# Kernel tuning notes

Hardware: AMD Instinct MI355X
Metric: run time of the kernel (lower is better)

The kernel has to match this reference:

```python
import jax, jax.numpy as jnp
import numpy as np

BS, C_IN, CTX, TGT = 2, 8, 1024, 96
D_MODEL, N_HEADS, D_FF, N_LAYERS = 256, 16, 1024, 4
PF, SF, PC, SC = 8, 4, 32, 16
NF = (CTX + SF - PF) // SF + 1   # 256 fine patches (incl. end-pad)
NC = (CTX + SC - PC) // SC + 1   # 64 coarse patches
TOTAL = NF + NC                  # 320
EPS = 1e-5
DK = D_MODEL // N_HEADS
SCALE = DK ** -0.5


def _patchify(z, plen, stride):
    # ReplicationPad1d((0, stride)) then unfold -> (bs, c, n_patches, plen)
    pad = jnp.broadcast_to(z[..., -1:], z.shape[:-1] + (stride,))
    zp = jnp.concatenate([z, pad], axis=-1)
    n = (zp.shape[-1] - plen) // stride + 1
    idx = np.arange(n)[:, None] * stride + np.arange(plen)[None, :]
    return zp[..., idx]


def _layernorm(x, s, b):
    m = x.mean(-1, keepdims=True)
    v = jnp.var(x, axis=-1, keepdims=True)
    return (x - m) * jax.lax.rsqrt(v + EPS) * s + b


def setup_inputs() -> dict:
    key = jax.random.key(0)
    ks = jax.random.split(key, 16)
    g = lambda k, shape: jax.random.normal(k, shape, jnp.float32) * 0.02
    return {
        "z": jax.random.normal(ks[0], (BS, C_IN, CTX), jnp.float32),
        "revin_w": jnp.ones((C_IN,), jnp.float32),
        "revin_b": jnp.zeros((C_IN,), jnp.float32),
        "Wf": g(ks[1], (PF, D_MODEL)), "bf": jnp.zeros((D_MODEL,), jnp.float32),
        "Wc": g(ks[2], (PC, D_MODEL)), "bc": jnp.zeros((D_MODEL,), jnp.float32),
        "W_pos": jax.random.uniform(ks[3], (TOTAL, D_MODEL), jnp.float32, -0.02, 0.02),
        "WQ": g(ks[4], (N_LAYERS, D_MODEL, D_MODEL)), "bQ": jnp.zeros((N_LAYERS, D_MODEL), jnp.float32),
        "WK": g(ks[5], (N_LAYERS, D_MODEL, D_MODEL)), "bK": jnp.zeros((N_LAYERS, D_MODEL), jnp.float32),
        "WV": g(ks[6], (N_LAYERS, D_MODEL, D_MODEL)), "bV": jnp.zeros((N_LAYERS, D_MODEL), jnp.float32),
        "WO": g(ks[7], (N_LAYERS, D_MODEL, D_MODEL)), "bO": jnp.zeros((N_LAYERS, D_MODEL), jnp.float32),
        "ln1_s": jnp.ones((N_LAYERS, D_MODEL), jnp.float32), "ln1_b": jnp.zeros((N_LAYERS, D_MODEL), jnp.float32),
        "ln2_s": jnp.ones((N_LAYERS, D_MODEL), jnp.float32), "ln2_b": jnp.zeros((N_LAYERS, D_MODEL), jnp.float32),
        "F1": g(ks[8], (N_LAYERS, D_MODEL, D_FF)), "c1": jnp.zeros((N_LAYERS, D_FF), jnp.float32),
        "F2": g(ks[9], (N_LAYERS, D_FF, D_MODEL)), "c2": jnp.zeros((N_LAYERS, D_MODEL), jnp.float32),
        "Wh": g(ks[10], (D_MODEL * TOTAL, TGT)), "bh": jnp.zeros((TGT,), jnp.float32),
    }


def reference(z, revin_w, revin_b, Wf, bf, Wc, bc, W_pos, WQ, bQ, WK, bK, WV, bV,
              WO, bO, ln1_s, ln1_b, ln2_s, ln2_b, F1, c1, F2, c2, Wh, bh):
    # RevIN norm over the time axis (last axis of (bs, c, T))
    mean = z.mean(-1, keepdims=True)
    std = jnp.sqrt(jnp.var(z, axis=-1, keepdims=True) + EPS)
    zn = (z - mean) / std * revin_w[None, :, None] + revin_b[None, :, None]

    # dual-scale patch embedding
    x_fine = _patchify(zn, PF, SF) @ Wf + bf      # (bs, c, NF, d)
    x_coarse = _patchify(zn, PC, SC) @ Wc + bc    # (bs, c, NC, d)
    x = jnp.concatenate([x_fine, x_coarse], axis=2)  # (bs, c, TOTAL, d)

    u = x.reshape(BS * C_IN, TOTAL, D_MODEL) + W_pos  # (B, S, d), B=bs*c

    # residual-score transformer encoder (post-norm)
    prev = None
    for l in range(N_LAYERS):
        q = (u @ WQ[l] + bQ[l]).reshape(-1, TOTAL, N_HEADS, DK).transpose(0, 2, 1, 3)
        k = (u @ WK[l] + bK[l]).reshape(-1, TOTAL, N_HEADS, DK).transpose(0, 2, 1, 3)
        v = (u @ WV[l] + bV[l]).reshape(-1, TOTAL, N_HEADS, DK).transpose(0, 2, 1, 3)
        s = jnp.einsum('bhqd,bhkd->bhqk', q, k) * SCALE
        if prev is not None:
            s = s + prev
        w = jax.nn.softmax(s, axis=-1)
        o = jnp.einsum('bhqk,bhkd->bhqd', w, v).transpose(0, 2, 1, 3).reshape(-1, TOTAL, D_MODEL)
        o = o @ WO[l] + bO[l]
        u = _layernorm(u + o, ln1_s[l], ln1_b[l])
        h = jax.nn.gelu(u @ F1[l] + c1[l], approximate=False) @ F2[l] + c2[l]
        u = _layernorm(u + h, ln2_s[l], ln2_b[l])
        prev = s

    # head: (bs, c, TOTAL, d) -> permute -> flatten(d, TOTAL) -> linear
    zz = u.reshape(BS, C_IN, TOTAL, D_MODEL).transpose(0, 1, 3, 2).reshape(BS, C_IN, D_MODEL * TOTAL)
    out = zz @ Wh + bh  # (bs, c, TGT)

    # RevIN denorm
    out = (out - revin_b[None, :, None]) / (revin_w[None, :, None] + EPS * EPS) * std + mean
    return out
```

## Files before the change

### kernel.cpp

```cpp
#include <hip/hip_runtime.h>
#include <math.h>

typedef unsigned short ushort;
typedef unsigned int uint;
typedef __attribute__((ext_vector_type(8))) short short8;
typedef __attribute__((ext_vector_type(4))) float f32x4;
typedef __attribute__((ext_vector_type(4))) ushort us4;

constexpr int BS = 2, C_IN = 8, CTX = 1024, TGT = 96;
constexpr int DM = 256, NH = 16, DFF = 1024, NL = 4;
constexpr int NF = 256, TOTAL = 320;
constexpr int NB = 16;
constexpr int DK = 16;
constexpr float EPS = 1e-5f;
constexpr float SCALE = 0.25f;
constexpr int KHEAD = DM * TOTAL;
constexpr int M = NB * TOTAL;

__device__ __forceinline__ ushort f2b(float x) {
    uint u = __float_as_uint(x);
    u += 0x7fff + ((u >> 16) & 1);
    return (ushort)(u >> 16);
}
__device__ __forceinline__ float bu2f(ushort x) { return __uint_as_float(((uint)x) << 16); }
__device__ __forceinline__ uint pack2(float a, float b) { return (uint)f2b(a) | ((uint)f2b(b) << 16); }

typedef __attribute__((address_space(3))) uint lds_u32;
typedef const __attribute__((address_space(1))) uint glb_u32;
__device__ __forceinline__ void ldst16(const void* g, void* l) {
    __builtin_amdgcn_global_load_lds((glb_u32*)g, (lds_u32*)l, 16, 0, 0);
}

__global__ void k_prep(const float* __restrict__ WQ, const float* __restrict__ WK,
                       const float* __restrict__ WV, const float* __restrict__ WO,
                       const float* __restrict__ F1, const float* __restrict__ F2,
                       const float* __restrict__ Wh,
                       ushort* __restrict__ Wtqkv, ushort* __restrict__ WtO,
                       ushort* __restrict__ Ft1, ushort* __restrict__ Ft2,
                       ushort* __restrict__ WhT2,
                       const float* __restrict__ z, const float* __restrict__ rw,
                       const float* __restrict__ rb, float* __restrict__ zn,
                       const float* __restrict__ bhv, float* __restrict__ outp,
                       float* __restrict__ scalef) {
    __shared__ ushort tile[32][33];
    __shared__ float rr1[16], rr2[16], bcast[2];
    int i = blockIdx.x;
    int tx = threadIdx.x, ty = threadIdx.y;
    if (i < 1024) {
        int zz = i >> 6, w = zz >> 2, l = zz & 3;
        const float* src = (w == 0 ? WQ : (w == 1 ? WK : (w == 2 ? WV : WO))) + l * 65536;
        ushort* dst = (w < 3) ? (Wtqkv + (size_t)l * 768 * 256 + w * 256 * 256)
                              : (WtO + (size_t)l * 65536);
        int c0 = (i & 7) * 32, r0 = ((i >> 3) & 7) * 32;
        tile[ty][tx] = f2b(src[(r0 + ty) * 256 + c0 + tx]);
        __syncthreads();
        dst[(c0 + ty) * 256 + r0 + tx] = tile[tx][ty];
    } else if (i < 2048) {
        int j = i - 1024, l = j >> 8;
        const float* src = F1 + (size_t)l * 262144;
        ushort* dst = Ft1 + (size_t)l * 262144;
        int c0 = (j & 31) * 32, r0 = ((j >> 5) & 7) * 32;
        tile[ty][tx] = f2b(src[(r0 + ty) * 1024 + c0 + tx]);
        __syncthreads();
        dst[(c0 + ty) * 256 + r0 + tx] = tile[tx][ty];
    } else if (i < 3072) {
        int j = i - 2048, l = j >> 8;
        const float* src = F2 + (size_t)l * 262144;
        ushort* dst = Ft2 + (size_t)l * 262144;
        int c0 = (j & 7) * 32, r0 = ((j >> 3) & 31) * 32;
        tile[ty][tx] = f2b(src[(r0 + ty) * 256 + c0 + tx]);
        __syncthreads();
        dst[(c0 + ty) * 1024 + r0 + tx] = tile[tx][ty];
    } else if (i < 10752) {
        int j = i - 3072;
        int t0 = (j % 3) * 32, rest = j / 3;
        int d0 = (rest & 7) * 32, pp = rest >> 3;
        tile[ty][tx] = f2b(Wh[((size_t)(d0 + ty) * 320 + pp) * 96 + t0 + tx]);
        __syncthreads();
        WhT2[(size_t)(t0 + ty) * KHEAD + pp * 256 + d0 + tx] = tile[tx][ty];
    } else {
        int bc = i - 10752;
        int tid = ty * 32 + tx;
        float x = z[bc * CTX + tid];
        float s1 = x, s2 = x * x;
#pragma unroll
        for (int off = 1; off < 64; off <<= 1) {
            s1 += __shfl_xor(s1, off);
            s2 += __shfl_xor(s2, off);
        }
        if ((tid & 63) == 0) { rr1[tid >> 6] = s1; rr2[tid >> 6] = s2; }
        __syncthreads();
        if (tid == 0) {
            float a1 = 0.f, a2 = 0.f;
            for (int k = 0; k < 16; k++) { a1 += rr1[k]; a2 += rr2[k]; }
            float m = a1 * (1.0f / CTX);
            float var = a2 * (1.0f / CTX) - m * m;
            float sd = sqrtf(var + EPS);
            bcast[0] = m; bcast[1] = sd;
        }
        __syncthreads();
        float m = bcast[0], sd = bcast[1];
        int c = bc & 7;
        float w = rw[c], bb = rb[c];
        zn[bc * CTX + tid] = (x - m) / sd * w + bb;
        if (tid < TGT) outp[bc * TGT + tid] = (bhv[tid] - bb) / (w + EPS * EPS) * sd + m;
        if (tid == 0) scalef[bc] = sd / (w + EPS * EPS);
    }
}

__global__ void k_embed(const float* __restrict__ zn, const float* __restrict__ Wf,
                        const float* __restrict__ bfv, const float* __restrict__ Wc,
                        const float* __restrict__ bcv, const float* __restrict__ Wpos,
                        ushort* __restrict__ u) {
    int bc = blockIdx.x / TOTAL, p = blockIdx.x % TOTAL, d = threadIdx.x;
    float acc;
    if (p < NF) {
        acc = bfv[d];
        int base = p * 4;
        for (int i = 0; i < 8; i++) {
            int idx = min(base + i, CTX - 1);
            acc += zn[bc * CTX + idx] * Wf[i * DM + d];
        }
    } else {
        int pc = p - NF;
        acc = bcv[d];
        int base = pc * 16;
        for (int i = 0; i < 32; i++) {
            int idx = min(base + i, CTX - 1);
            acc += zn[bc * CTX + idx] * Wc[i * DM + d];
        }
    }
    acc += Wpos[p * DM + d];
    u[(bc * TOTAL + p) * DM + d] = f2b(acc);
}

template <int GELU, int QKV>
__global__ __launch_bounds__(256) void k_gemm_mfma(const ushort* __restrict__ A,
                                                   const ushort* __restrict__ Wt,
                                                   const float* __restrict__ b0,
                                                   const float* __restrict__ b1,
                                                   const float* __restrict__ b2,
                                                   ushort* __restrict__ C,
                                                   ushort* __restrict__ C2,
                                                   int Mm, int N, int K) {
    __shared__ ushort As[64][32];
    __shared__ ushort Bs[64][32];
    int tid = threadIdx.x;
    int wave = tid >> 6, lane = tid & 63;
    int quad = lane >> 4, l16 = lane & 15;
    int m0 = blockIdx.y * 64, n0 = blockIdx.x * 64;

    f32x4 acc[4];
#pragma unroll
    for (int nt = 0; nt < 4; nt++) acc[nt] = (f32x4){0.f, 0.f, 0.f, 0.f};

    int srow = wave * 16 + (lane >> 2);
    int sc = (lane & 3) ^ ((srow >> 1) & 3);
    ushort* AsW = &As[wave * 16][0];
    ushort* BsW = &Bs[wave * 16][0];
    const ushort* Ag = &A[(size_t)(m0 + srow) * K + sc * 8];
    const ushort* Bg = &Wt[(size_t)(n0 + srow) * K + sc * 8];
    int rchunk = (quad ^ ((l16 >> 1) & 3)) * 8;

    for (int k0 = 0; k0 < K; k0 += 32) {
        ldst16(Ag + k0, AsW);
        ldst16(Bg + k0, BsW);
        __syncthreads();
        short8 af = *(const short8*)&As[wave * 16 + l16][rchunk];
#pragma unroll
        for (int nt = 0; nt < 4; nt++) {
            short8 bf = *(const short8*)&Bs[nt * 16 + l16][rchunk];
            acc[nt] = __builtin_amdgcn_mfma_f32_16x16x32_bf16(af, bf, acc[nt], 0, 0, 0);
        }
        __syncthreads();
    }
#pragma unroll
    for (int nt = 0; nt < 4; nt++) {
        int col = n0 + nt * 16 + l16;
        float bi;
        if (QKV) {
            int bs = (n0 + nt * 16) >> 8;
            const float* bp = bs == 0 ? b0 : (bs == 1 ? b1 : b2);
            bi = bp[col & 255];
        } else {
            bi = b0[col];
        }
#pragma unroll
        for (int r = 0; r < 4; r++) {
            int rowm = m0 + wave * 16 + quad * 4 + r;
            float vv = acc[nt][r] + bi;
            if (GELU) vv = vv * 0.5f * (1.0f + erff(vv * 0.70710678118f));
            if (QKV) {
                int bs = col >> 8;
                ushort* dst = (bs == 2) ? (C2 + (size_t)rowm * DM)
                                        : (C + (size_t)bs * (M * DM) + (size_t)rowm * DM);
                dst[col & 255] = f2b(vv);
            } else {
                C[(size_t)rowm * N + col] = f2b(vv);
            }
        }
    }
}

__global__ __launch_bounds__(256) void k_gemm_ln16(const ushort* __restrict__ A,
                                                   const ushort* __restrict__ Wt,
                                                   const float* __restrict__ bias,
                                                   const float* __restrict__ ls,
                                                   const float* __restrict__ lb,
                                                   ushort* __restrict__ u, int K) {
    __shared__ ushort As[16][32];
    __shared__ ushort Bs[256][32];
    __shared__ float ps1[16][4], ps2[16][4];
    int tid = threadIdx.x;
    int wave = tid >> 6, lane = tid & 63;
    int quad = lane >> 4, l16 = lane & 15;
    int m0 = blockIdx.x * 16;

    f32x4 acc[4];
#pragma unroll
    for (int nt = 0; nt < 4; nt++) acc[nt] = (f32x4){0.f, 0.f, 0.f, 0.f};

    int brow = wave * 16 + (lane >> 2);
    int bc_swz = (lane & 3) ^ ((brow >> 1) & 3);
    const ushort* Bg0 = &Wt[(size_t)brow * K + bc_swz * 8];
    ushort* BsW0 = &Bs[wave * 16][0];
    int ar = lane >> 2;
    int ac = (lane & 3) ^ ((ar >> 1) & 3);
    const ushort* Ag = &A[(size_t)(m0 + ar) * K + ac * 8];
    int rchunk = (quad ^ ((l16 >> 1) & 3)) * 8;

    for (int k0 = 0; k0 < K; k0 += 32) {
        if (tid < 64) ldst16(Ag + k0, &As[0][0]);
#pragma unroll
        for (int i = 0; i < 4; i++)
            ldst16(Bg0 + (size_t)i * 64 * K + k0, BsW0 + i * 64 * 32);
        __syncthreads();
        short8 af = *(const short8*)&As[l16][rchunk];
#pragma unroll
        for (int nt = 0; nt < 4; nt++) {
            short8 bf = *(const short8*)&Bs[wave * 64 + nt * 16 + l16][rchunk];
            acc[nt] = __builtin_amdgcn_mfma_f32_16x16x32_bf16(af, bf, acc[nt], 0, 0, 0);
        }
        __syncthreads();
    }
    float xv[4][4];
#pragma unroll
    for (int r = 0; r < 4; r++) {
        int rowg = m0 + quad * 4 + r;
        float s1 = 0.f, s2 = 0.f;
#pragma unroll
        for (int nt = 0; nt < 4; nt++) {
            int col = wave * 64 + nt * 16 + l16;
            float x = acc[nt][r] + bias[col] + bu2f(u[(size_t)rowg * DM + col]);
            xv[r][nt] = x; s1 += x; s2 += x * x;
        }
        s1 += __shfl_xor(s1, 1); s2 += __shfl_xor(s2, 1);
        s1 += __shfl_xor(s1, 2); s2 += __shfl_xor(s2, 2);
        s1 += __shfl_xor(s1, 4); s2 += __shfl_xor(s2, 4);
        s1 += __shfl_xor(s1, 8); s2 += __shfl_xor(s2, 8);
        if (l16 == 0) { ps1[quad * 4 + r][wave] = s1; ps2[quad * 4 + r][wave] = s2; }
    }
    __syncthreads();
#pragma unroll
    for (int r = 0; r < 4; r++) {
        int rowl = quad * 4 + r, rowg = m0 + rowl;
        float s1 = ps1[rowl][0] + ps1[rowl][1] + ps1[rowl][2] + ps1[rowl][3];
        float s2 = ps2[rowl][0] + ps2[rowl][1] + ps2[rowl][2] + ps2[rowl][3];
        float m = s1 * (1.0f / DM);
        float var = s2 * (1.0f / DM) - m * m;
        float rs = rsqrtf(var + EPS);
#pragma unroll
        for (int nt = 0; nt < 4; nt++) {
            int col = wave * 64 + nt * 16 + l16;
            u[(size_t)rowg * DM + col] = f2b((xv[r][nt] - m) * rs * ls[col] + lb[col]);
        }
    }
}

__global__ __launch_bounds__(256, 4) void k_attn(const ushort* __restrict__ qk, const ushort* __restrict__ vm,
                                                 ushort* __restrict__ ao, int nj) {
    __shared__ ushort sh[10240];
    uint* sh32 = (uint*)sh;
    int bh = blockIdx.x, b = bh >> 4, h = bh & 15;
    int i0 = blockIdx.y * 64;
    int t = threadIdx.x, wave = t >> 6, lane = t & 63, quad = lane >> 4, l16 = lane & 15;
    const short8 zero8 = (short8){0, 0, 0, 0, 0, 0, 0, 0};

    f32x4 acc[20];
#pragma unroll
    for (int nt = 0; nt < 20; nt++) acc[nt] = (f32x4){0.f, 0.f, 0.f, 0.f};

    for (int idx = t; idx < 320; idx += 256) {
        int jp = idx >> 1, dh = idx & 1;
        int j = jp * 2;
        uint4 a = *(const uint4*)&vm[((size_t)b * TOTAL + j) * DM + h * DK + dh * 8];
        uint4 bb = *(const uint4*)&vm[((size_t)b * TOTAL + j + 1) * DM + h * DK + dh * 8];
        const ushort* ap = (const ushort*)&a;
        const ushort* bp = (const ushort*)&bb;
        int jr = j & 31;
        int q = (jr & 15) >> 2, jj = ((jr >> 4) << 2) + (jr & 3);
        int base = 5120 + ((j >> 5) * 4 + q) * 128 + jj;
#pragma unroll
        for (int dd = 0; dd < 8; dd++) {
            int d = dh * 8 + dd;
            uint val = (uint)ap[dd] | ((uint)bp[dd] << 16);
            sh32[(base + d * 8) >> 1] = val;
        }
    }

    for (int jl = 0; jl < nj; jl++) {
        const ushort* qm = qk + (size_t)(2 * jl) * M * DM;
        const ushort* km = qm + (size_t)M * DM;
        for (int idx = t; idx < 640; idx += 256) {
            int j = idx >> 1, half = idx & 1;
            short8 kv = *(const short8*)&km[((size_t)b * TOTAL + j) * DM + h * DK + half * 8];
            int jt = j >> 4, jln = j & 15;
            *(short8*)&sh[((jt * 2 + half) * 16 + jln) * 8] = kv;
        }
        short8 qf = zero8;
        if (quad < 2) qf = *(const short8*)&qm[((size_t)b * TOTAL + i0 + wave * 16 + l16) * DM + h * DK + quad * 8];
        __syncthreads();
#pragma unroll
        for (int nt = 0; nt < 20; nt++) {
            short8 kf = *(const short8*)&sh[((nt * 2 + (quad & 1)) * 16 + l16) * 8];
            acc[nt] = __builtin_amdgcn_mfma_f32_16x16x32_bf16(kf, qf, acc[nt], 0, 0, 0);
        }
        __syncthreads();
    }

    float mx = -1e30f;
#pragma unroll
    for (int nt = 0; nt < 20; nt++)
#pragma unroll
        for (int r = 0; r < 4; r++) { acc[nt][r] *= SCALE; mx = fmaxf(mx, acc[nt][r]); }
    mx = fmaxf(mx, __shfl_xor(mx, 16));
    mx = fmaxf(mx, __shfl_xor(mx, 32));
    float sum = 0.f;
#pragma unroll
    for (int nt = 0; nt < 20; nt++)
#pragma unroll
        for (int r = 0; r < 4; r++) { acc[nt][r] = __expf(acc[nt][r] - mx); sum += acc[nt][r]; }
    sum += __shfl_xor(sum, 16);
    sum += __shfl_xor(sum, 32);
    float inv = 1.f / sum;
#pragma unroll
    for (int nt = 0; nt < 20; nt++)
#pragma unroll
        for (int r = 0; r < 4; r++) acc[nt][r] *= inv;

    f32x4 oacc = (f32x4){0.f, 0.f, 0.f, 0.f};
#pragma unroll
    for (int jt2 = 0; jt2 < 10; jt2++) {
        short8 vt = *(const short8*)&sh[5120 + ((jt2 * 4 + quad) * 16 + l16) * 8];
        union { short8 v; uint u[4]; } pf;
        pf.u[0] = pack2(acc[2 * jt2][0], acc[2 * jt2][1]);
        pf.u[1] = pack2(acc[2 * jt2][2], acc[2 * jt2][3]);
        pf.u[2] = pack2(acc[2 * jt2 + 1][0], acc[2 * jt2 + 1][1]);
        pf.u[3] = pack2(acc[2 * jt2 + 1][2], acc[2 * jt2 + 1][3]);
        oacc = __builtin_amdgcn_mfma_f32_16x16x32_bf16(vt, pf.v, oacc, 0, 0, 0);
    }
    us4 ov4 = (us4){f2b(oacc[0]), f2b(oacc[1]), f2b(oacc[2]), f2b(oacc[3])};
    *(us4*)&ao[((size_t)b * TOTAL + i0 + wave * 16 + l16) * DM + h * DK + quad * 4] = ov4;
}

__global__ __launch_bounds__(256) void k_head(const ushort* __restrict__ u, const ushort* __restrict__ WhT2,
                                              const float* __restrict__ scalef, float* __restrict__ out) {
    int t0 = blockIdx.x * 16;
    int wave = threadIdx.x >> 6, lane = threadIdx.x & 63;
    int quad = lane >> 4, l16 = lane & 15;
    int chunk = blockIdx.y * 4 + wave;
    int kbeg = chunk * 1024;
    f32x4 acc = (f32x4){0.f, 0.f, 0.f, 0.f};
    const ushort* za = &u[(size_t)l16 * KHEAD + quad * 8];
    const ushort* wb = &WhT2[(size_t)(t0 + l16) * KHEAD + quad * 8];
#pragma unroll 4
    for (int k = kbeg; k < kbeg + 1024; k += 32) {
        short8 af = *(const short8*)&za[k];
        short8 bf = *(const short8*)&wb[k];
        acc = __builtin_amdgcn_mfma_f32_16x16x32_bf16(af, bf, acc, 0, 0, 0);
    }
#pragma unroll
    for (int r = 0; r < 4; r++) {
        int bcr = quad * 4 + r;
        atomicAdd(&out[bcr * TGT + t0 + l16], acc[r] * scalef[bcr]);
    }
}

extern "C" void kernel_launch(void* const* d_in, const int* in_sizes, int n_in,
                              void* d_out, int out_size, void* d_ws, size_t ws_size,
                              hipStream_t stream) {
    const float* z       = (const float*)d_in[0];
    const float* revin_w = (const float*)d_in[1];
    const float* revin_b = (const float*)d_in[2];
    const float* Wf      = (const float*)d_in[3];
    const float* bfv     = (const float*)d_in[4];
    const float* Wc      = (const float*)d_in[5];
    const float* bcv     = (const float*)d_in[6];
    const float* Wpos    = (const float*)d_in[7];
    const float* WQ      = (const float*)d_in[8];
    const float* bQ      = (const float*)d_in[9];
    const float* WK      = (const float*)d_in[10];
    const float* bK      = (const float*)d_in[11];
    const float* WV      = (const float*)d_in[12];
    const float* bV      = (const float*)d_in[13];
    const float* WO      = (const float*)d_in[14];
    const float* bO      = (const float*)d_in[15];
    const float* ln1s    = (const float*)d_in[16];
    const float* ln1b    = (const float*)d_in[17];
    const float* ln2s    = (const float*)d_in[18];
    const float* ln2b    = (const float*)d_in[19];
    const float* F1      = (const float*)d_in[20];
    const float* c1      = (const float*)d_in[21];
    const float* F2      = (const float*)d_in[22];
    const float* c2      = (const float*)d_in[23];
    const float* Wh      = (const float*)d_in[24];
    const float* bh      = (const float*)d_in[25];
    float* out = (float*)d_out;

    char* p = (char*)d_ws;
    float* scalef = (float*)p;   p += 16 * 4;
    p = (char*)(((size_t)p + 255) & ~255ull);
    float* zn = (float*)p;       p += NB * CTX * 4;
    ushort* u     = (ushort*)p;  p += (size_t)M * DM * 2;
    ushort* qkbuf = (ushort*)p;  p += (size_t)NL * 2 * M * DM * 2;
    ushort* vbuf  = (ushort*)p;  p += (size_t)M * DM * 2;
    ushort* ax    = (ushort*)p;  p += (size_t)M * DM * 2;
    ushort* hbuf  = (ushort*)p;  p += (size_t)M * DFF * 2;
    ushort* Wtqkv = (ushort*)p;  p += (size_t)NL * 768 * 256 * 2;
    ushort* WtO   = (ushort*)p;  p += (size_t)NL * 256 * 256 * 2;
    ushort* Ft1   = (ushort*)p;  p += (size_t)NL * 1024 * 256 * 2;
    ushort* Ft2   = (ushort*)p;  p += (size_t)NL * 256 * 1024 * 2;
    ushort* WhT2  = (ushort*)p;  p += (size_t)TGT * KHEAD * 2;

    k_prep<<<10768, dim3(32, 32), 0, stream>>>(WQ, WK, WV, WO, F1, F2, Wh,
                                               Wtqkv, WtO, Ft1, Ft2, WhT2,
                                               z, revin_w, revin_b, zn,
                                               bh, out, scalef);
    k_embed<<<NB * TOTAL, 256, 0, stream>>>(zn, Wf, bfv, Wc, bcv, Wpos, u);

    for (int l = 0; l < NL; l++) {
        k_gemm_mfma<0, 1><<<dim3(12, 80), 256, 0, stream>>>(
            u, Wtqkv + (size_t)l * 768 * 256, bQ + l * DM, bK + l * DM, bV + l * DM,
            qkbuf + (size_t)l * 2 * M * DM, vbuf, M, 768, 256);
        k_attn<<<dim3(NB * NH, 5), 256, 0, stream>>>(qkbuf, vbuf, ax, l + 1);
        k_gemm_ln16<<<M / 16, 256, 0, stream>>>(
            ax, WtO + (size_t)l * 65536, bO + l * DM, ln1s + l * DM, ln1b + l * DM, u, 256);
        k_gemm_mfma<1, 0><<<dim3(16, 80), 256, 0, stream>>>(
            u, Ft1 + (size_t)l * 262144, c1 + l * DFF, c1, c1, hbuf, hbuf, M, 1024, 256);
        k_gemm_ln16<<<M / 16, 256, 0, stream>>>(
            hbuf, Ft2 + (size_t)l * 262144, c2 + l * DM, ln2s + l * DM, ln2b + l * DM, u, 1024);
    }

    k_head<<<dim3(TGT / 16, 20), 256, 0, stream>>>(u, WhT2, scalef, out);
}
```

Baseline: 459.4 us.

## Double-buffer LDS tiles in GEMM kernels and attention K staging

Both MFMA GEMM kernels now use two LDS buffers. The next K-slice is loaded with global_load_lds while the current slice feeds the MFMAs, and each step ends with a single waitcnt+barrier instead of two __syncthreads. The attention kernel alternates K staging between two LDS regions so the trailing barrier per layer-iteration can be dropped. This hides global-load latency and cuts barrier count, at the cost of doubled LDS use, which may reduce occupancy.

```diff
diff --git a/kernel.cpp b/kernel.cpp
--- a/kernel.cpp
+++ b/kernel.cpp
@@ -30,6 +30,8 @@
 __device__ __forceinline__ void ldst16(const void* g, void* l) {
     __builtin_amdgcn_global_load_lds((glb_u32*)g, (lds_u32*)l, 16, 0, 0);
 }
+
+#define PIPE_BARRIER() asm volatile("s_waitcnt vmcnt(0)\n\ts_barrier" ::: "memory")
 
 __global__ void k_prep(const float* __restrict__ WQ, const float* __restrict__ WK,
                        const float* __restrict__ WV, const float* __restrict__ WO,
@@ -143,8 +145,8 @@
                                                    ushort* __restrict__ C,
                                                    ushort* __restrict__ C2,
                                                    int Mm, int N, int K) {
-    __shared__ ushort As[64][32];
-    __shared__ ushort Bs[64][32];
+    __shared__ ushort As[2][64][32];
+    __shared__ ushort Bs[2][64][32];
     int tid = threadIdx.x;
     int wave = tid >> 6, lane = tid & 63;
     int quad = lane >> 4, l16 = lane & 15;
@@ -156,23 +158,29 @@
 
     int srow = wave * 16 + (lane >> 2);
     int sc = (lane & 3) ^ ((srow >> 1) & 3);
-    ushort* AsW = &As[wave * 16][0];
-    ushort* BsW = &Bs[wave * 16][0];
     const ushort* Ag = &A[(size_t)(m0 + srow) * K + sc * 8];
     const ushort* Bg = &Wt[(size_t)(n0 + srow) * K + sc * 8];
     int rchunk = (quad ^ ((l16 >> 1) & 3)) * 8;
 
-    for (int k0 = 0; k0 < K; k0 += 32) {
-        ldst16(Ag + k0, AsW);
-        ldst16(Bg + k0, BsW);
-        __syncthreads();
-        short8 af = *(const short8*)&As[wave * 16 + l16][rchunk];
+    ldst16(Ag, &As[0][wave * 16][0]);
+    ldst16(Bg, &Bs[0][wave * 16][0]);
+    PIPE_BARRIER();
+
+    int nstep = K >> 5;
+    int cur = 0;
+    for (int t = 0; t < nstep; t++) {
+        if (t + 1 < nstep) {
+            ldst16(Ag + (t + 1) * 32, &As[cur ^ 1][wave * 16][0]);
+            ldst16(Bg + (t + 1) * 32, &Bs[cur ^ 1][wave * 16][0]);
+        }
+        short8 af = *(const short8*)&As[cur][wave * 16 + l16][rchunk];
 #pragma unroll
         for (int nt = 0; nt < 4; nt++) {
-            short8 bf = *(const short8*)&Bs[nt * 16 + l16][rchunk];
+            short8 bf = *(const short8*)&Bs[cur][nt * 16 + l16][rchunk];
             acc[nt] = __builtin_amdgcn_mfma_f32_16x16x32_bf16(af, bf, acc[nt], 0, 0, 0);
         }
-        __syncthreads();
+        PIPE_BARRIER();
+        cur ^= 1;
     }
 #pragma unroll
     for (int nt = 0; nt < 4; nt++) {
@@ -208,8 +216,8 @@
                                                    const float* __restrict__ ls,
                                                    const float* __restrict__ lb,
                                                    ushort* __restrict__ u, int K) {
-    __shared__ ushort As[16][32];
-    __shared__ ushort Bs[256][32];
+    __shared__ ushort As[2][16][32];
+    __shared__ ushort Bs[2][256][32];
     __shared__ float ps1[16][4], ps2[16][4];
     int tid = threadIdx.x;
     int wave = tid >> 6, lane = tid & 63;
@@ -223,25 +231,34 @@
     int brow = wave * 16 + (lane >> 2);
     int bc_swz = (lane & 3) ^ ((brow >> 1) & 3);
     const ushort* Bg0 = &Wt[(size_t)brow * K + bc_swz * 8];
-    ushort* BsW0 = &Bs[wave * 16][0];
     int ar = lane >> 2;
     int ac = (lane & 3) ^ ((ar >> 1) & 3);
     const ushort* Ag = &A[(size_t)(m0 + ar) * K + ac * 8];
     int rchunk = (quad ^ ((l16 >> 1) & 3)) * 8;
 
-    for (int k0 = 0; k0 < K; k0 += 32) {
-        if (tid < 64) ldst16(Ag + k0, &As[0][0]);
-#pragma unroll
-        for (int i = 0; i < 4; i++)
-            ldst16(Bg0 + (size_t)i * 64 * K + k0, BsW0 + i * 64 * 32);
-        __syncthreads();
-        short8 af = *(const short8*)&As[l16][rchunk];
+    if (tid < 64) ldst16(Ag, &As[0][0][0]);
+#pragma unroll
+    for (int i = 0; i < 4; i++)
+        ldst16(Bg0 + (size_t)i * 64 * K, &Bs[0][i * 64 + wave * 16][0]);
+    PIPE_BARRIER();
+
+    int nstep = K >> 5;
+    int cur = 0;
+    for (int t = 0; t < nstep; t++) {
+        if (t + 1 < nstep) {
+            if (tid < 64) ldst16(Ag + (t + 1) * 32, &As[cur ^ 1][0][0]);
+#pragma unroll
+            for (int i = 0; i < 4; i++)
+                ldst16(Bg0 + (size_t)i * 64 * K + (t + 1) * 32, &Bs[cur ^ 1][i * 64 + wave * 16][0]);
+        }
+        short8 af = *(const short8*)&As[cur][l16][rchunk];
 #pragma unroll
         for (int nt = 0; nt < 4; nt++) {
-            short8 bf = *(const short8*)&Bs[wave * 64 + nt * 16 + l16][rchunk];
+            short8 bf = *(const short8*)&Bs[cur][wave * 64 + nt * 16 + l16][rchunk];
             acc[nt] = __builtin_amdgcn_mfma_f32_16x16x32_bf16(af, bf, acc[nt], 0, 0, 0);
         }
-        __syncthreads();
+        PIPE_BARRIER();
+        cur ^= 1;
     }
     float xv[4][4];
 #pragma unroll
@@ -279,7 +296,7 @@
 
 __global__ __launch_bounds__(256, 4) void k_attn(const ushort* __restrict__ qk, const ushort* __restrict__ vm,
                                                  ushort* __restrict__ ao, int nj) {
-    __shared__ ushort sh[10240];
+    __shared__ ushort sh[15360];
     uint* sh32 = (uint*)sh;
     int bh = blockIdx.x, b = bh >> 4, h = bh & 15;
     int i0 = blockIdx.y * 64;
@@ -299,7 +316,7 @@
         const ushort* bp = (const ushort*)&bb;
         int jr = j & 31;
         int q = (jr & 15) >> 2, jj = ((jr >> 4) << 2) + (jr & 3);
-        int base = 5120 + ((j >> 5) * 4 + q) * 128 + jj;
+        int base = 10240 + ((j >> 5) * 4 + q) * 128 + jj;
 #pragma unroll
         for (int dd = 0; dd < 8; dd++) {
             int d = dh * 8 + dd;
@@ -311,21 +328,21 @@
     for (int jl = 0; jl < nj; jl++) {
         const ushort* qm = qk + (size_t)(2 * jl) * M * DM;
         const ushort* km = qm + (size_t)M * DM;
+        int kb = (jl & 1) * 5120;
         for (int idx = t; idx < 640; idx += 256) {
             int j = idx >> 1, half = idx & 1;
             short8 kv = *(const short8*)&km[((size_t)b * TOTAL + j) * DM + h * DK + half * 8];
             int jt = j >> 4, jln = j & 15;
-            *(short8*)&sh[((jt * 2 + half) * 16 + jln) * 8] = kv;
+            *(short8*)&sh[kb + ((jt * 2 + half) * 16 + jln) * 8] = kv;
         }
         short8 qf = zero8;
         if (quad < 2) qf = *(const short8*)&qm[((size_t)b * TOTAL + i0 + wave * 16 + l16) * DM + h * DK + quad * 8];
         __syncthreads();
 #pragma unroll
         for (int nt = 0; nt < 20; nt++) {
-            short8 kf = *(const short8*)&sh[((nt * 2 + (quad & 1)) * 16 + l16) * 8];
+            short8 kf = *(const short8*)&sh[kb + ((nt * 2 + (quad & 1)) * 16 + l16) * 8];
             acc[nt] = __builtin_amdgcn_mfma_f32_16x16x32_bf16(kf, qf, acc[nt], 0, 0, 0);
         }
-        __syncthreads();
     }
 
     float mx = -1e30f;
@@ -351,7 +368,7 @@
     f32x4 oacc = (f32x4){0.f, 0.f, 0.f, 0.f};
 #pragma unroll
     for (int jt2 = 0; jt2 < 10; jt2++) {
-        short8 vt = *(const short8*)&sh[5120 + ((jt2 * 4 + quad) * 16 + l16) * 8];
+        short8 vt = *(const short8*)&sh[10240 + ((jt2 * 4 + quad) * 16 + l16) * 8];
         union { short8 v; uint u[4]; } pf;
         pf.u[0] = pack2(acc[2 * jt2][0], acc[2 * jt2][1]);
         pf.u[1] = pack2(acc[2 * jt2][2], acc[2 * jt2][3]);
```

Measured after the change: 460.3 us. No clear change (+0.2%).
